# Kernel tuning notes

Hardware: AMD Instinct MI355X
Metric: run time of the kernel (lower is better)

Reference implementation:

```python
import jax, jax.numpy as jnp
import numpy as np

B = 512          # batch
SIZE_IN = 1024   # input features
SIZE_OUT = 256   # output features
NUM_Q = 16       # quantiles


def setup_inputs() -> dict:
    key = jax.random.key(0)
    k1, k2, k3, k4 = jax.random.split(key, 4)
    x = jax.random.normal(k1, (B, SIZE_IN), dtype=jnp.float32)
    indices = jax.random.randint(k2, (B, SIZE_IN), 0, NUM_Q, dtype=jnp.int64)
    # param_index table: row (q*SIZE_IN + j) holds a SIZE_OUT weight vector
    param_table = jax.random.normal(k3, (NUM_Q * SIZE_IN, SIZE_OUT), dtype=jnp.float32)
    bias = jax.random.normal(k4, (SIZE_OUT,), dtype=jnp.float32)
    return {"x": x, "indices": indices, "param_table": param_table, "bias": bias}


def reference(x, indices, param_table, bias):
    size_in = x.shape[1]
    # flat row index into the quantile-indexed table: q*size_in + feature_pos
    flat_idx = indices * size_in + jnp.arange(size_in, dtype=indices.dtype)[None, :]  # [B, In]
    gathered = param_table[flat_idx]  # [B, In, Out] gather
    # scale each gathered weight vector by the scalar input and reduce over features
    out = jnp.einsum('bi,bio->bo', x, gathered)  # [B, Out]
    return out + bias
```

## Files before the change

### kernel.cpp

```cpp
#include <hip/hip_runtime.h>
#include <stdint.h>


constexpr int SIZE_IN  = 1024;
constexpr int SIZE_OUT = 256;
constexpr int BATCH    = 512;
constexpr int NUM_Q    = 16;
constexpr int TM = 16;
constexpr int TN = 16;

typedef short short8   __attribute__((ext_vector_type(8)));
typedef float floatx4  __attribute__((ext_vector_type(4)));

__device__ inline uint32_t pack2bf(float lo, float hi) {
    uint32_t a = __float_as_uint(lo) + 0x8000u;
    uint32_t b = __float_as_uint(hi) + 0x8000u;
    return __builtin_amdgcn_perm(b, a, 0x07060302);
}

__global__ __launch_bounds__(512, 4)
void idxlin_qsplit2(const float* __restrict__ x,
                    const int*   __restrict__ idx,
                    const float* __restrict__ table,
                    const float* __restrict__ bias,
                    float*       __restrict__ out)
{
    __shared__ uint16_t x_lds[TM * 1024];
    __shared__ uint32_t i_lds[TM * 128];
    __shared__ float    red[8][64][4];

    const int tid = threadIdx.x;

    const int h    = blockIdx.x & 7;
    const int half = (blockIdx.x >> 3) & 1;
    const int bt   = blockIdx.x >> 4;
    const int nh   = h * 2 + half;
    const int b0   = bt * TM;
    const int n0   = nh * TN;

    const float4* x4 = reinterpret_cast<const float4*>(x + b0 * SIZE_IN);
    char* xb = reinterpret_cast<char*>(x_lds);
    #pragma unroll
    for (int it = 0; it < 8; ++it) {
        const int u   = it * 512 + tid;
        const int row = u >> 8;
        const int c8  = u & 255;
        const float4 xv = x4[u];
        uint2 d;
        d.x = pack2bf(xv.x, xv.y);
        d.y = pack2bf(xv.z, xv.w);
        const int byte = row * 2048 + ((c8 * 8) ^ ((row & 7) << 4));
        *reinterpret_cast<uint2*>(xb + byte) = d;
    }

    const int4* i4 = reinterpret_cast<const int4*>(idx + b0 * SIZE_IN);
    char* ib = reinterpret_cast<char*>(i_lds);
    #pragma unroll
    for (int it = 0; it < 4; ++it) {
        const int u   = it * 512 + tid;
        const int row = u >> 7;
        const int c32 = u & 127;
        const int4 a = i4[2 * u];
        const int4 b = i4[2 * u + 1];
        const uint32_t n =  (uint32_t)a.x        | ((uint32_t)a.y << 4)
                         | ((uint32_t)a.z << 8)  | ((uint32_t)a.w << 12)
                         | ((uint32_t)b.x << 16) | ((uint32_t)b.y << 20)
                         | ((uint32_t)b.z << 24) | ((uint32_t)b.w << 28);
        const int byte = row * 512 + ((c32 * 4) ^ ((row & 15) << 2));
        *reinterpret_cast<uint32_t*>(ib + byte) = n;
    }
    __syncthreads();

    const int lane  = tid & 63;
    const int w     = tid >> 6;
    const int nlane = lane & 15;
    const int quad  = lane >> 4;
    const int q0    = w * 2;

    const char* xrow = xb + nlane * 2048;
    const char* irow = ib + nlane * 512;
    const int   sx   = (nlane & 7) << 4;
    const int   si   = (nlane & 15) << 2;

    const float* bq0 = table + ((q0 * SIZE_IN + quad * 8) * SIZE_OUT) + n0 + nlane;
    const float* bq1 = bq0 + SIZE_IN * SIZE_OUT;

    floatx4 acc = {0.f, 0.f, 0.f, 0.f};

    #pragma unroll 2
    for (int kb = 0; kb < SIZE_IN / 32; ++kb) {
        union { uint32_t u[4]; short8 s; } ar;
        ar.s = *reinterpret_cast<const short8*>(xrow + ((kb * 64 + quad * 16) ^ sx));
        const uint32_t nib = *reinterpret_cast<const uint32_t*>(
                                 irow + ((kb * 16 + quad * 4) ^ si));
        uint32_t en[8];
        #pragma unroll
        for (int j = 0; j < 8; ++j) en[j] = (nib >> (4 * j)) & 15u;

        #pragma unroll
        for (int qq = 0; qq < 2; ++qq) {
            const uint32_t q = (uint32_t)(q0 + qq);
            const float* bp = qq ? bq1 : bq0;

            float wv[8];
            #pragma unroll
            for (int j = 0; j < 8; ++j) wv[j] = bp[j * SIZE_OUT];

            union { uint32_t u[4]; short8 s; } af;
            #pragma unroll
            for (int p = 0; p < 4; ++p) {
                const uint32_t msk = (en[2*p]     == q ? 0x0000FFFFu : 0u)
                                   | (en[2*p + 1] == q ? 0xFFFF0000u : 0u);
                af.u[p] = ar.u[p] & msk;
            }

            union { uint32_t u[4]; short8 s; } bf;
            bf.u[0] = pack2bf(wv[0], wv[1]);
            bf.u[1] = pack2bf(wv[2], wv[3]);
            bf.u[2] = pack2bf(wv[4], wv[5]);
            bf.u[3] = pack2bf(wv[6], wv[7]);

            acc = __builtin_amdgcn_mfma_f32_16x16x32_bf16(af.s, bf.s, acc, 0, 0, 0);
        }
        bq0 += 32 * SIZE_OUT;
        bq1 += 32 * SIZE_OUT;
    }

    #pragma unroll
    for (int rr = 0; rr < 4; ++rr) red[w][lane][rr] = acc[rr];
    __syncthreads();

    if (tid < 256) {
        const int l  = tid >> 2;
        const int rr = tid & 3;
        float s = red[0][l][rr];
        #pragma unroll
        for (int ww = 1; ww < 8; ++ww) s += red[ww][l][rr];
        const int row = b0 + (l >> 4) * 4 + rr;
        const int col = n0 + (l & 15);
        out[row * SIZE_OUT + col] = s + bias[col];
    }
}

extern "C" void kernel_launch(void* const* d_in, const int* in_sizes, int n_in,
                              void* d_out, int out_size, void* d_ws, size_t ws_size,
                              hipStream_t stream) {
    const float* x     = (const float*)d_in[0];
    const int*   idx   = (const int*)d_in[1];
    const float* table = (const float*)d_in[2];
    const float* bias  = (const float*)d_in[3];
    float*       out   = (float*)d_out;
    (void)d_ws; (void)ws_size;

    idxlin_qsplit2<<<dim3((BATCH / TM) * (SIZE_OUT / TN)), dim3(512), 0, stream>>>(
        x, idx, table, bias, out);
}
```

Baseline: 110.5 us.

## Use 1024-thread blocks with one quantile per wave and prefetch weights

Doubles the block to 16 waves so each wave handles a single quantile instead of two, which halves the serial MFMA work per wave. It also adds register double-buffering of the next k-step's table loads so global latency overlaps the mask and MFMA work. The cross-wave reduction grows to 16 partials. The larger blocks raise register pressure, since launch bounds of (1024, 8) limit registers per thread, and the bigger shared reduction buffer can reduce occupancy.

```diff
diff --git a/kernel.cpp b/kernel.cpp
--- a/kernel.cpp
+++ b/kernel.cpp
@@ -18,16 +18,16 @@
     return __builtin_amdgcn_perm(b, a, 0x07060302);
 }
 
-__global__ __launch_bounds__(512, 4)
-void idxlin_qsplit2(const float* __restrict__ x,
-                    const int*   __restrict__ idx,
-                    const float* __restrict__ table,
-                    const float* __restrict__ bias,
-                    float*       __restrict__ out)
+__global__ __launch_bounds__(1024, 8)
+void idxlin_q1(const float* __restrict__ x,
+               const int*   __restrict__ idx,
+               const float* __restrict__ table,
+               const float* __restrict__ bias,
+               float*       __restrict__ out)
 {
     __shared__ uint16_t x_lds[TM * 1024];
     __shared__ uint32_t i_lds[TM * 128];
-    __shared__ float    red[8][64][4];
+    __shared__ float    red[16][64][4];
 
     const int tid = threadIdx.x;
 
@@ -41,8 +41,8 @@
     const float4* x4 = reinterpret_cast<const float4*>(x + b0 * SIZE_IN);
     char* xb = reinterpret_cast<char*>(x_lds);
     #pragma unroll
-    for (int it = 0; it < 8; ++it) {
-        const int u   = it * 512 + tid;
+    for (int it = 0; it < 4; ++it) {
+        const int u   = it * 1024 + tid;
         const int row = u >> 8;
         const int c8  = u & 255;
         const float4 xv = x4[u];
@@ -56,8 +56,8 @@
     const int4* i4 = reinterpret_cast<const int4*>(idx + b0 * SIZE_IN);
     char* ib = reinterpret_cast<char*>(i_lds);
     #pragma unroll
-    for (int it = 0; it < 4; ++it) {
-        const int u   = it * 512 + tid;
+    for (int it = 0; it < 2; ++it) {
+        const int u   = it * 1024 + tid;
         const int row = u >> 7;
         const int c32 = u & 127;
         const int4 a = i4[2 * u];
@@ -75,55 +75,59 @@
     const int w     = tid >> 6;
     const int nlane = lane & 15;
     const int quad  = lane >> 4;
-    const int q0    = w * 2;
+    const uint32_t q = (uint32_t)w;
 
     const char* xrow = xb + nlane * 2048;
     const char* irow = ib + nlane * 512;
     const int   sx   = (nlane & 7) << 4;
     const int   si   = (nlane & 15) << 2;
 
-    const float* bq0 = table + ((q0 * SIZE_IN + quad * 8) * SIZE_OUT) + n0 + nlane;
-    const float* bq1 = bq0 + SIZE_IN * SIZE_OUT;
+    const float* bp = table + (((int)q * SIZE_IN + quad * 8) * SIZE_OUT) + n0 + nlane;
 
     floatx4 acc = {0.f, 0.f, 0.f, 0.f};
 
-    #pragma unroll 2
+    float wv[8];
+    #pragma unroll
+    for (int j = 0; j < 8; ++j) wv[j] = bp[j * SIZE_OUT];
+
+    #pragma unroll 4
     for (int kb = 0; kb < SIZE_IN / 32; ++kb) {
+        const float* bn = bp + 32 * SIZE_OUT;
+        float wn[8];
+        if (kb < SIZE_IN / 32 - 1) {
+            #pragma unroll
+            for (int j = 0; j < 8; ++j) wn[j] = bn[j * SIZE_OUT];
+        } else {
+            #pragma unroll
+            for (int j = 0; j < 8; ++j) wn[j] = 0.f;
+        }
+
         union { uint32_t u[4]; short8 s; } ar;
         ar.s = *reinterpret_cast<const short8*>(xrow + ((kb * 64 + quad * 16) ^ sx));
         const uint32_t nib = *reinterpret_cast<const uint32_t*>(
                                  irow + ((kb * 16 + quad * 4) ^ si));
-        uint32_t en[8];
+
+        union { uint32_t u[4]; short8 s; } af;
         #pragma unroll
-        for (int j = 0; j < 8; ++j) en[j] = (nib >> (4 * j)) & 15u;
+        for (int p = 0; p < 4; ++p) {
+            const uint32_t e0 = (nib >> (8 * p)) & 15u;
+            const uint32_t e1 = (nib >> (8 * p + 4)) & 15u;
+            const uint32_t msk = (e0 == q ? 0x0000FFFFu : 0u)
+                               | (e1 == q ? 0xFFFF0000u : 0u);
+            af.u[p] = ar.u[p] & msk;
+        }
+
+        union { uint32_t u[4]; short8 s; } bf;
+        bf.u[0] = pack2bf(wv[0], wv[1]);
+        bf.u[1] = pack2bf(wv[2], wv[3]);
+        bf.u[2] = pack2bf(wv[4], wv[5]);
+        bf.u[3] = pack2bf(wv[6], wv[7]);
+
+        acc = __builtin_amdgcn_mfma_f32_16x16x32_bf16(af.s, bf.s, acc, 0, 0, 0);
 
         #pragma unroll
-        for (int qq = 0; qq < 2; ++qq) {
-            const uint32_t q = (uint32_t)(q0 + qq);
-            const float* bp = qq ? bq1 : bq0;
-
-            float wv[8];
-            #pragma unroll
-            for (int j = 0; j < 8; ++j) wv[j] = bp[j * SIZE_OUT];
-
-            union { uint32_t u[4]; short8 s; } af;
-            #pragma unroll
-            for (int p = 0; p < 4; ++p) {
-                const uint32_t msk = (en[2*p]     == q ? 0x0000FFFFu : 0u)
-                                   | (en[2*p + 1] == q ? 0xFFFF0000u : 0u);
-                af.u[p] = ar.u[p] & msk;
-            }
-
-            union { uint32_t u[4]; short8 s; } bf;
-            bf.u[0] = pack2bf(wv[0], wv[1]);
-            bf.u[1] = pack2bf(wv[2], wv[3]);
-            bf.u[2] = pack2bf(wv[4], wv[5]);
-            bf.u[3] = pack2bf(wv[6], wv[7]);
-
-            acc = __builtin_amdgcn_mfma_f32_16x16x32_bf16(af.s, bf.s, acc, 0, 0, 0);
-        }
-        bq0 += 32 * SIZE_OUT;
-        bq1 += 32 * SIZE_OUT;
+        for (int j = 0; j < 8; ++j) wv[j] = wn[j];
+        bp = bn;
     }
 
     #pragma unroll
@@ -135,7 +139,7 @@
         const int rr = tid & 3;
         float s = red[0][l][rr];
         #pragma unroll
-        for (int ww = 1; ww < 8; ++ww) s += red[ww][l][rr];
+        for (int ww = 1; ww < 16; ++ww) s += red[ww][l][rr];
         const int row = b0 + (l >> 4) * 4 + rr;
         const int col = n0 + (l & 15);
         out[row * SIZE_OUT + col] = s + bias[col];
@@ -152,6 +156,6 @@
     float*       out   = (float*)d_out;
     (void)d_ws; (void)ws_size;
 
-    idxlin_qsplit2<<<dim3((BATCH / TM) * (SIZE_OUT / TN)), dim3(512), 0, stream>>>(
+    idxlin_q1<<<dim3((BATCH / TM) * (SIZE_OUT / TN)), dim3(1024), 0, stream>>>(
         x, idx, table, bias, out);
 }
```

After: 111.2 us. Within noise of the previous version (+0.7%).
